# Kernel optimization log

Measured on AMD Instinct MI355X. Metric: run time of the kernel, lower is better.

Reference implementation:

```python
import jax, jax.numpy as jnp
import numpy as np


def setup_inputs() -> dict:
    key = jax.random.key(0)
    k1, k2 = jax.random.split(key)
    latents = jax.random.normal(k1, (32, 1024, 64), dtype=jnp.float32)
    codebook = jax.random.normal(k2, (8192, 64), dtype=jnp.float32)
    return {"latents": latents, "codebook": codebook}


def reference(latents, codebook):
    # Faithful to: cdist(latents_flat, codebook) -> argmin(dim=1) -> reshape(B, L)
    B, L, D = latents.shape
    x = latents.reshape(-1, D)                         # (N, D)
    x2 = jnp.sum(x * x, axis=1, keepdims=True)         # (N, 1)
    c2 = jnp.sum(codebook * codebook, axis=1)          # (K,)
    # (N, K) distance matrix, then argmin reduction
    d2 = x2 - 2.0 * (x @ codebook.T) + c2[None, :]
    indices = jnp.argmin(d2, axis=1)                   # (N,)
    return indices.reshape(B, L)
```

## Files before the change

### kernel.cpp

```cpp
#include <hip/hip_runtime.h>
#include <stdint.h>


#define N_TOTAL 32768
#define K_CODES 8192
#define EPS_GAP 0.008f

typedef __attribute__((ext_vector_type(4)))  float  floatx4;
typedef __attribute__((ext_vector_type(8)))  __bf16 bf16x8;

#define O_C2    0u
#define O_CBSW  32768u
#define O_PS1   2129920u
#define O_PS2   2654208u
#define O_PI1   3178496u
#define WS_NEED 4096256u

__device__ __forceinline__ void load_lds16(const void* g, void* l) {
    __builtin_amdgcn_global_load_lds(
        (const __attribute__((address_space(1))) unsigned int*)g,
        (__attribute__((address_space(3))) unsigned int*)l, 16, 0, 0);
}

__global__ __launch_bounds__(256) void vq_prep(
    const float4* __restrict__ cb, uint4* __restrict__ cbSw,
    float* __restrict__ c2) {
    __shared__ float red[256];
    const int m = threadIdx.x & 31, g = threadIdx.x >> 5;
    const int rb = blockIdx.x;
    float4 a = cb[(size_t)(rb * 32 + m) * 16 + g * 2];
    float4 b = cb[(size_t)(rb * 32 + m) * 16 + g * 2 + 1];
    float x[8] = {a.x, a.y, a.z, a.w, b.x, b.y, b.z, b.w};
    bf16x8 hv, lv;
    float ss = 0.f;
#pragma unroll
    for (int i = 0; i < 8; ++i) {
        float v  = x[i];
        __bf16 hb = (__bf16)v;
        float r  = v - (float)hb;
        hv[i] = hb;
        lv[i] = (__bf16)r;
        ss += v * v;
    }
    cbSw[(size_t)rb * 512 + g * 32 + m]       = __builtin_bit_cast(uint4, hv);
    cbSw[(size_t)rb * 512 + (8 + g) * 32 + m] = __builtin_bit_cast(uint4, lv);
    red[threadIdx.x] = ss;
    __syncthreads();
    if (threadIdx.x < 32) {
        float s = 0.f;
#pragma unroll
        for (int gg = 0; gg < 8; ++gg) s += red[threadIdx.x + 32 * gg];
        c2[rb * 32 + threadIdx.x] = s;
    }
}

__global__ __launch_bounds__(256, 4) void vq_mfma(
    const float4* __restrict__ lat, const uint4* __restrict__ cbSw,
    const float* __restrict__ c2,
    float* __restrict__ pS1, float* __restrict__ pS2, int* __restrict__ pI1) {
    __shared__ uint4 Bs[2][1024];
    const int tid = threadIdx.x;
    const int wr = tid >> 6, lane = tid & 63;
    const int c16 = lane & 15, h4 = lane >> 4;

    const int q0 = blockIdx.x * 128 + wr * 32 + c16;
    bf16x8 aH[2][2], aL[2][2];
#pragma unroll
    for (int qt = 0; qt < 2; ++qt)
#pragma unroll
    for (int c = 0; c < 2; ++c) {
        float4 v0 = lat[(size_t)(q0 + qt * 16) * 16 + c * 8 + h4 * 2];
        float4 v1 = lat[(size_t)(q0 + qt * 16) * 16 + c * 8 + h4 * 2 + 1];
        float x[8] = {v0.x, v0.y, v0.z, v0.w, v1.x, v1.y, v1.z, v1.w};
#pragma unroll
        for (int j = 0; j < 8; ++j) {
            float v  = x[j];
            __bf16 hb = (__bf16)v;
            aH[qt][c][j] = hb;
            aL[qt][c][j] = (__bf16)(v - (float)hb);
        }
    }

    float t1[2][4], t2[2][4]; int i1[2][4];
#pragma unroll
    for (int qt = 0; qt < 2; ++qt)
#pragma unroll
    for (int r = 0; r < 4; ++r) { t1[qt][r] = -3e38f; t2[qt][r] = -3e38f; i1[qt][r] = 0; }

    const int kBase = blockIdx.y * 2048;
    const uint4* srcBase = cbSw + ((size_t)(kBase >> 5) << 9);
    const float* c2g = c2 + kBase + c16;

    float ccCur[4], ccNxt[4];
#pragma unroll
    for (int T = 0; T < 4; ++T) ccCur[T] = c2g[T * 16];
#pragma unroll
    for (int i = 0; i < 4; ++i)
        load_lds16(&srcBase[wr * 256 + i * 64 + lane], &Bs[0][wr * 256 + i * 64]);
    __syncthreads();

    int cur = 0;
    for (int stage = 0; stage < 32; ++stage) {
        if (stage + 1 < 32) {
            const uint4* sp = srcBase + (size_t)(stage + 1) * 1024;
#pragma unroll
            for (int i = 0; i < 4; ++i)
                load_lds16(&sp[wr * 256 + i * 64 + lane],
                           &Bs[cur ^ 1][wr * 256 + i * 64]);
#pragma unroll
            for (int T = 0; T < 4; ++T)
                ccNxt[T] = c2g[(stage + 1) * 64 + T * 16];
        }

        const int colBase = kBase + stage * 64 + c16;

        __builtin_amdgcn_s_setprio(1);
#pragma unroll
        for (int T = 0; T < 4; ++T) {
            const float nn = -0.5f * ccCur[T];
            const int col = colBase + T * 16;
            const int bb = (T >> 1) * 512 + (T & 1) * 16 + c16 + h4 * 32;
            bf16x8 bH0 = __builtin_bit_cast(bf16x8, Bs[cur][bb]);
            bf16x8 bH1 = __builtin_bit_cast(bf16x8, Bs[cur][bb + 128]);
            bf16x8 bL0 = __builtin_bit_cast(bf16x8, Bs[cur][bb + 256]);
            bf16x8 bL1 = __builtin_bit_cast(bf16x8, Bs[cur][bb + 384]);
#pragma unroll
            for (int qt = 0; qt < 2; ++qt) {
                floatx4 acc = {nn, nn, nn, nn};
                acc = __builtin_amdgcn_mfma_f32_16x16x32_bf16(aH[qt][0], bH0, acc, 0, 0, 0);
                acc = __builtin_amdgcn_mfma_f32_16x16x32_bf16(aH[qt][1], bH1, acc, 0, 0, 0);
                acc = __builtin_amdgcn_mfma_f32_16x16x32_bf16(aL[qt][0], bH0, acc, 0, 0, 0);
                acc = __builtin_amdgcn_mfma_f32_16x16x32_bf16(aL[qt][1], bH1, acc, 0, 0, 0);
                acc = __builtin_amdgcn_mfma_f32_16x16x32_bf16(aH[qt][0], bL0, acc, 0, 0, 0);
                acc = __builtin_amdgcn_mfma_f32_16x16x32_bf16(aH[qt][1], bL1, acc, 0, 0, 0);
#pragma unroll
                for (int r = 0; r < 4; ++r) {
                    float a = acc[r];
                    bool gt = a > t1[qt][r];
                    t2[qt][r] = __builtin_amdgcn_fmed3f(a, t1[qt][r], t2[qt][r]);
                    t1[qt][r] = fmaxf(t1[qt][r], a);
                    i1[qt][r] = gt ? col : i1[qt][r];
                }
            }
        }
        __builtin_amdgcn_s_setprio(0);

        __syncthreads();
#pragma unroll
        for (int T = 0; T < 4; ++T) ccCur[T] = ccNxt[T];
        cur ^= 1;
    }

#pragma unroll
    for (int mask = 1; mask <= 8; mask <<= 1) {
#pragma unroll
        for (int qt = 0; qt < 2; ++qt)
#pragma unroll
        for (int r = 0; r < 4; ++r) {
            float o1 = __shfl_xor(t1[qt][r], mask);
            float o2 = __shfl_xor(t2[qt][r], mask);
            int   oi = __shfl_xor(i1[qt][r], mask);
            float n2 = fmaxf(fmaxf(t2[qt][r], o2), fminf(t1[qt][r], o1));
            bool take = (o1 > t1[qt][r]) || (o1 == t1[qt][r] && oi < i1[qt][r]);
            t1[qt][r] = take ? o1 : t1[qt][r];
            i1[qt][r] = take ? oi : i1[qt][r];
            t2[qt][r] = n2;
        }
    }

    if (c16 == 0) {
        const int o0 = blockIdx.y * N_TOTAL;
#pragma unroll
        for (int qt = 0; qt < 2; ++qt) {
            const int qb = blockIdx.x * 128 + wr * 32 + qt * 16 + h4 * 4;
#pragma unroll
            for (int r = 0; r < 4; ++r) {
                pS1[o0 + qb + r] = -2.f * t1[qt][r];
                pS2[o0 + qb + r] = -2.f * t2[qt][r];
                pI1[o0 + qb + r] = i1[qt][r];
            }
        }
    }
}

__global__ __launch_bounds__(256) void vq_tail(
    const float4* __restrict__ lat, const float* __restrict__ cbf,
    const float* __restrict__ c2,
    const float* __restrict__ pS1, const float* __restrict__ pS2,
    const int* __restrict__ pI1, int* __restrict__ out) {
    __shared__ unsigned char fqv[132];
    __shared__ unsigned char fmk[132];
    __shared__ int fcnt;
    __shared__ float qv[64];
    __shared__ float redS[256];
    __shared__ int   redI[256];

    const int tid = threadIdx.x;
    if (tid == 0) fcnt = 0;
    __syncthreads();

    if (tid < 128) {
        const int q = blockIdx.x * 128 + tid;
        float g1 = 3e38f, g2 = 3e38f;
        int   gi = 0x7FFFFFFF;
        float s2v[4];
#pragma unroll
        for (int p = 0; p < 4; ++p) {
            float s1p = pS1[p * N_TOTAL + q];
            float s2p = pS2[p * N_TOTAL + q];
            int   i1p = pI1[p * N_TOTAL + q];
            s2v[p] = s2p;
            bool take = (s1p < g1) || (s1p == g1 && i1p < gi);
            g2 = fminf(g2, fminf(s2p, take ? g1 : s1p));
            if (take) { g1 = s1p; gi = i1p; }
        }
        out[q] = gi;
        if (g2 - g1 < EPS_GAP) {
            int msk = 0;
#pragma unroll
            for (int p = 0; p < 4; ++p)
                if (s2v[p] - g1 < EPS_GAP) msk |= (1 << p);
            int e = atomicAdd(&fcnt, 1);
            fqv[e] = (unsigned char)tid;
            fmk[e] = (unsigned char)msk;
        }
    }
    __syncthreads();

    const int ne = fcnt;
    for (int e = 0; e < ne; ++e) {
        const int lq = fqv[e];
        const int gq = blockIdx.x * 128 + lq;
        const int msk = fmk[e];
        if (tid < 16) {
            float4 v = lat[(size_t)gq * 16 + tid];
            *(float4*)&qv[tid * 4] = v;
        }
        __syncthreads();

        float best = 3e38f; int bi = 0x7FFFFFFF;
        if (tid < 4 && !((msk >> tid) & 1)) {
            const int k = pI1[tid * N_TOTAL + gq];
            const float4* cp = (const float4*)&cbf[(size_t)k * 64];
            float dot = 0.f;
#pragma unroll
            for (int d4 = 0; d4 < 16; ++d4) {
                float4 cv = cp[d4];
                dot += qv[d4 * 4 + 0] * cv.x + qv[d4 * 4 + 1] * cv.y
                     + qv[d4 * 4 + 2] * cv.z + qv[d4 * 4 + 3] * cv.w;
            }
            float s = c2[k] - 2.f * dot;
            if (s < best || (s == best && k < bi)) { best = s; bi = k; }
        }
#pragma unroll
        for (int p = 0; p < 4; ++p) if ((msk >> p) & 1) {
            for (int j = tid; j < 2048; j += 256) {
                const int k = p * 2048 + j;
                const float4* cp = (const float4*)&cbf[(size_t)k * 64];
                float dot = 0.f;
#pragma unroll
                for (int d4 = 0; d4 < 16; ++d4) {
                    float4 cv = cp[d4];
                    dot += qv[d4 * 4 + 0] * cv.x + qv[d4 * 4 + 1] * cv.y
                         + qv[d4 * 4 + 2] * cv.z + qv[d4 * 4 + 3] * cv.w;
                }
                float s = c2[k] - 2.f * dot;
                if (s < best || (s == best && k < bi)) { best = s; bi = k; }
            }
        }
        redS[tid] = best; redI[tid] = bi;
        __syncthreads();
        for (int s = 128; s > 0; s >>= 1) {
            if (tid < s) {
                float os = redS[tid + s]; int oi = redI[tid + s];
                if (os < redS[tid] || (os == redS[tid] && oi < redI[tid])) {
                    redS[tid] = os; redI[tid] = oi;
                }
            }
            __syncthreads();
        }
        if (tid == 0) out[gq] = redI[0];
        __syncthreads();
    }
}

#define BM 128
#define BN 128
#define PAD 68

__global__ void vq_norms_fb(const float4* __restrict__ cb, float* __restrict__ c2) {
    int t = blockIdx.x * 256 + threadIdx.x;
    int r = t >> 2, p = t & 3;
    float s = 0.f;
#pragma unroll
    for (int i = 0; i < 4; ++i) {
        float4 v = cb[r * 16 + p * 4 + i];
        s += v.x * v.x + v.y * v.y + v.z * v.z + v.w * v.w;
    }
    s += __shfl_xor(s, 1);
    s += __shfl_xor(s, 2);
    if (p == 0) c2[r] = s;
}

__global__ __launch_bounds__(256) void vq_fp32(
    const float4* __restrict__ lat, const float4* __restrict__ cb,
    const float* __restrict__ c2, int ktPer,
    int* __restrict__ outIdx, float* __restrict__ partS, int* __restrict__ partI,
    int writePartial) {
    __shared__ float As[BM][PAD];
    __shared__ float Bsf[BN][PAD];
    __shared__ float c2s[BN];
    const int tid = threadIdx.x;
    const int tx = tid & 15;
    const int ty = tid >> 4;
    const int nBase = blockIdx.x * BM;
    const int kt0 = blockIdx.y * ktPer;
    const int ktN = kt0 + ktPer;
#pragma unroll
    for (int r = 0; r < 8; ++r) {
        int f = tid + 256 * r;
        int mm = f >> 4, d4 = f & 15;
        float4 v = lat[(size_t)(nBase + mm) * 16 + d4];
        *(float4*)&As[mm][d4 * 4] = v;
    }
    float best[8]; int bidx[8];
#pragma unroll
    for (int ii = 0; ii < 8; ++ii) { best[ii] = 3e38f; bidx[ii] = 0; }
    for (int kt = kt0; kt < ktN; ++kt) {
        const int kbase = kt * BN;
        __syncthreads();
#pragma unroll
        for (int r = 0; r < 8; ++r) {
            int f = tid + 256 * r;
            int k = f >> 4, d4 = f & 15;
            float4 v = cb[(size_t)(kbase + k) * 16 + d4];
            *(float4*)&Bsf[k][d4 * 4] = v;
        }
        if (tid < BN) c2s[tid] = c2[kbase + tid];
        __syncthreads();
        float acc[8][8];
#pragma unroll
        for (int ii = 0; ii < 8; ++ii)
#pragma unroll
            for (int jj = 0; jj < 8; ++jj) acc[ii][jj] = 0.f;
#pragma unroll 4
        for (int d4 = 0; d4 < 16; ++d4) {
            float4 a[8], b[8];
#pragma unroll
            for (int ii = 0; ii < 8; ++ii) a[ii] = *(const float4*)&As[tx + 16 * ii][d4 * 4];
#pragma unroll
            for (int jj = 0; jj < 8; ++jj) b[jj] = *(const float4*)&Bsf[ty + 16 * jj][d4 * 4];
#pragma unroll
            for (int ii = 0; ii < 8; ++ii)
#pragma unroll
                for (int jj = 0; jj < 8; ++jj)
                    acc[ii][jj] += a[ii].x * b[jj].x + a[ii].y * b[jj].y
                                 + a[ii].z * b[jj].z + a[ii].w * b[jj].w;
        }
#pragma unroll
        for (int jj = 0; jj < 8; ++jj) {
            int k = kbase + ty + 16 * jj;
            float cc = c2s[ty + 16 * jj];
#pragma unroll
            for (int ii = 0; ii < 8; ++ii) {
                float s = cc - 2.f * acc[ii][jj];
                if (s < best[ii]) { best[ii] = s; bidx[ii] = k; }
            }
        }
    }
    __syncthreads();
    float* redS = &As[0][0];
    int*   redI = (int*)&Bsf[0][0];
#pragma unroll
    for (int ii = 0; ii < 8; ++ii) {
        int mm = tx + 16 * ii;
        redS[ty * BM + mm] = best[ii];
        redI[ty * BM + mm] = bidx[ii];
    }
    __syncthreads();
    if (tid < BM) {
        int mm = tid;
        float bs = redS[mm]; int bi = redI[mm];
#pragma unroll
        for (int t = 1; t < 16; ++t) {
            float s = redS[t * BM + mm]; int i = redI[t * BM + mm];
            if (s < bs || (s == bs && i < bi)) { bs = s; bi = i; }
        }
        int n = nBase + mm;
        if (writePartial) { partS[blockIdx.y * N_TOTAL + n] = bs; partI[blockIdx.y * N_TOTAL + n] = bi; }
        else outIdx[n] = bi;
    }
}

__global__ void vq_merge_fb(const float* __restrict__ partS, const int* __restrict__ partI,
                            int* __restrict__ out) {
    int n = blockIdx.x * 256 + threadIdx.x;
    float s0 = partS[n], s1 = partS[N_TOTAL + n];
    int   i0 = partI[n], i1 = partI[N_TOTAL + n];
    out[n] = (s1 < s0) ? i1 : i0;
}

extern "C" void kernel_launch(void* const* d_in, const int* in_sizes, int n_in,
                              void* d_out, int out_size, void* d_ws, size_t ws_size,
                              hipStream_t stream) {
    const float4* lat = (const float4*)d_in[0];
    const float4* cb  = (const float4*)d_in[1];
    int* out = (int*)d_out;
    char* ws = (char*)d_ws;

    if (ws_size >= WS_NEED) {
        float* c2   = (float*)(ws + O_C2);
        uint4* cbSw = (uint4*)(ws + O_CBSW);
        float* pS1  = (float*)(ws + O_PS1);
        float* pS2  = (float*)(ws + O_PS2);
        int*   pI1  = (int*)(ws + O_PI1);

        vq_prep<<<256, 256, 0, stream>>>(cb, cbSw, c2);
        vq_mfma<<<dim3(256, 4), 256, 0, stream>>>(lat, cbSw, c2, pS1, pS2, pI1);
        vq_tail<<<256, 256, 0, stream>>>(lat, (const float*)cb, c2, pS1, pS2, pI1, out);
    } else {
        float* c2 = (float*)ws;
        vq_norms_fb<<<128, 256, 0, stream>>>(cb, c2);
        const size_t needSplit = 32768u + 2u * N_TOTAL * 4u + 2u * N_TOTAL * 4u + 64u;
        if (ws_size >= needSplit) {
            float* partS = (float*)(ws + 32768);
            int*   partI = (int*)(ws + 32768 + 2 * N_TOTAL * 4);
            dim3 grid(N_TOTAL / BM, 2);
            vq_fp32<<<grid, 256, 0, stream>>>(lat, cb, c2, (K_CODES / BN) / 2, out, partS, partI, 1);
            vq_merge_fb<<<N_TOTAL / 256, 256, 0, stream>>>(partS, partI, out);
        } else {
            dim3 grid(N_TOTAL / BM, 1);
            vq_fp32<<<grid, 256, 0, stream>>>(lat, cb, c2, K_CODES / BN, out, nullptr, nullptr, 0);
        }
    }
}
```

Before: 195.1 us.

## Load codebook fragments directly from global into registers, drop LDS staging

The kernel no longer stages codebook tiles into shared memory with async global-to-LDS copies and block barriers. Each wave now loads its B fragments straight from global memory into registers, prefetching one 16-column step ahead, and the loop runs over 128 fine steps. This removes the LDS traffic and the per-stage __syncthreads. In exchange, every wave in the block fetches the same codebook data separately, so global and L2 traffic rises, and the single-step register prefetch may not hide load latency.

```diff
diff --git a/kernel.cpp b/kernel.cpp
--- a/kernel.cpp
+++ b/kernel.cpp
@@ -58,7 +58,6 @@
     const float4* __restrict__ lat, const uint4* __restrict__ cbSw,
     const float* __restrict__ c2,
     float* __restrict__ pS1, float* __restrict__ pS2, int* __restrict__ pI1) {
-    __shared__ uint4 Bs[2][1024];
     const int tid = threadIdx.x;
     const int wr = tid >> 6, lane = tid & 63;
     const int c16 = lane & 15, h4 = lane >> 4;
@@ -88,67 +87,55 @@
     for (int r = 0; r < 4; ++r) { t1[qt][r] = -3e38f; t2[qt][r] = -3e38f; i1[qt][r] = 0; }
 
     const int kBase = blockIdx.y * 2048;
-    const uint4* srcBase = cbSw + ((size_t)(kBase >> 5) << 9);
+    const uint4* sB = cbSw + ((size_t)(kBase >> 5) << 9);
     const float* c2g = c2 + kBase + c16;
-
-    float ccCur[4], ccNxt[4];
-#pragma unroll
-    for (int T = 0; T < 4; ++T) ccCur[T] = c2g[T * 16];
-#pragma unroll
-    for (int i = 0; i < 4; ++i)
-        load_lds16(&srcBase[wr * 256 + i * 64 + lane], &Bs[0][wr * 256 + i * 64]);
-    __syncthreads();
-
-    int cur = 0;
-    for (int stage = 0; stage < 32; ++stage) {
-        if (stage + 1 < 32) {
-            const uint4* sp = srcBase + (size_t)(stage + 1) * 1024;
-#pragma unroll
-            for (int i = 0; i < 4; ++i)
-                load_lds16(&sp[wr * 256 + i * 64 + lane],
-                           &Bs[cur ^ 1][wr * 256 + i * 64]);
-#pragma unroll
-            for (int T = 0; T < 4; ++T)
-                ccNxt[T] = c2g[(stage + 1) * 64 + T * 16];
-        }
-
-        const int colBase = kBase + stage * 64 + c16;
+    const int fb = c16 + h4 * 32;
+
+
+    uint4 b0, b1, b2, b3;
+    {
+        const uint4* p = sB + fb;
+        b0 = p[0]; b1 = p[128]; b2 = p[256]; b3 = p[384];
+    }
+    float ccCur = c2g[0];
+
+#pragma unroll 2
+    for (int step = 0; step < 128; ++step) {
+        const int s1 = (step + 1 < 128) ? (step + 1) : 127;
+        const uint4* p = sB + ((s1 >> 2) << 10) + ((s1 & 2) << 8) + ((s1 & 1) << 4) + fb;
+        uint4 n0 = p[0], n1 = p[128], n2 = p[256], n3 = p[384];
+        float ccN = c2g[((s1 >> 2) << 6) + ((s1 & 3) << 4)];
+
+        const int col = kBase + ((step >> 2) << 6) + ((step & 3) << 4) + c16;
+        const float nn = -0.5f * ccCur;
+        bf16x8 bH0 = __builtin_bit_cast(bf16x8, b0);
+        bf16x8 bH1 = __builtin_bit_cast(bf16x8, b1);
+        bf16x8 bL0 = __builtin_bit_cast(bf16x8, b2);
+        bf16x8 bL1 = __builtin_bit_cast(bf16x8, b3);
 
         __builtin_amdgcn_s_setprio(1);
 #pragma unroll
-        for (int T = 0; T < 4; ++T) {
-            const float nn = -0.5f * ccCur[T];
-            const int col = colBase + T * 16;
-            const int bb = (T >> 1) * 512 + (T & 1) * 16 + c16 + h4 * 32;
-            bf16x8 bH0 = __builtin_bit_cast(bf16x8, Bs[cur][bb]);
-            bf16x8 bH1 = __builtin_bit_cast(bf16x8, Bs[cur][bb + 128]);
-            bf16x8 bL0 = __builtin_bit_cast(bf16x8, Bs[cur][bb + 256]);
-            bf16x8 bL1 = __builtin_bit_cast(bf16x8, Bs[cur][bb + 384]);
-#pragma unroll
-            for (int qt = 0; qt < 2; ++qt) {
-                floatx4 acc = {nn, nn, nn, nn};
-                acc = __builtin_amdgcn_mfma_f32_16x16x32_bf16(aH[qt][0], bH0, acc, 0, 0, 0);
-                acc = __builtin_amdgcn_mfma_f32_16x16x32_bf16(aH[qt][1], bH1, acc, 0, 0, 0);
-                acc = __builtin_amdgcn_mfma_f32_16x16x32_bf16(aL[qt][0], bH0, acc, 0, 0, 0);
-                acc = __builtin_amdgcn_mfma_f32_16x16x32_bf16(aL[qt][1], bH1, acc, 0, 0, 0);
-                acc = __builtin_amdgcn_mfma_f32_16x16x32_bf16(aH[qt][0], bL0, acc, 0, 0, 0);
-                acc = __builtin_amdgcn_mfma_f32_16x16x32_bf16(aH[qt][1], bL1, acc, 0, 0, 0);
-#pragma unroll
-                for (int r = 0; r < 4; ++r) {
-                    float a = acc[r];
-                    bool gt = a > t1[qt][r];
-                    t2[qt][r] = __builtin_amdgcn_fmed3f(a, t1[qt][r], t2[qt][r]);
-                    t1[qt][r] = fmaxf(t1[qt][r], a);
-                    i1[qt][r] = gt ? col : i1[qt][r];
-                }
+        for (int qt = 0; qt < 2; ++qt) {
+            floatx4 acc = {nn, nn, nn, nn};
+            acc = __builtin_amdgcn_mfma_f32_16x16x32_bf16(aH[qt][0], bH0, acc, 0, 0, 0);
+            acc = __builtin_amdgcn_mfma_f32_16x16x32_bf16(aH[qt][1], bH1, acc, 0, 0, 0);
+            acc = __builtin_amdgcn_mfma_f32_16x16x32_bf16(aL[qt][0], bH0, acc, 0, 0, 0);
+            acc = __builtin_amdgcn_mfma_f32_16x16x32_bf16(aL[qt][1], bH1, acc, 0, 0, 0);
+            acc = __builtin_amdgcn_mfma_f32_16x16x32_bf16(aH[qt][0], bL0, acc, 0, 0, 0);
+            acc = __builtin_amdgcn_mfma_f32_16x16x32_bf16(aH[qt][1], bL1, acc, 0, 0, 0);
+#pragma unroll
+            for (int r = 0; r < 4; ++r) {
+                float a = acc[r];
+                bool gt = a > t1[qt][r];
+                t2[qt][r] = __builtin_amdgcn_fmed3f(a, t1[qt][r], t2[qt][r]);
+                t1[qt][r] = fmaxf(t1[qt][r], a);
+                i1[qt][r] = gt ? col : i1[qt][r];
             }
         }
         __builtin_amdgcn_s_setprio(0);
 
-        __syncthreads();
-#pragma unroll
-        for (int T = 0; T < 4; ++T) ccCur[T] = ccNxt[T];
-        cur ^= 1;
+        b0 = n0; b1 = n1; b2 = n2; b3 = n3;
+        ccCur = ccN;
     }
 
 #pragma unroll
```

New measurement: 203.6 us. 4.4% more time.
